# Kernel tuning notes

Measured on AMD Instinct MI355X. Metric: run time of the kernel, lower is better.

## Reference

```python
import jax, jax.numpy as jnp
import numpy as np

B, M, N, E = 64, 100, 6400, 102400   # graphs, nodes/graph, total nodes, edges
H, D, EMB, IMG, NC = 4, 512, 768, 1024, 2
HD = H * D
EPS = 1e-5


def _bn2(x, g, b, m, v):
    # BatchNorm1d eval mode on [B, C]
    return (x - m) / jnp.sqrt(v + EPS) * g + b


def _bn3(x, g, b, m, v):
    # BatchNorm1d eval mode on [B, C, L] -> channel dim is axis 1 (node index)
    return (x - m[None, :, None]) / jnp.sqrt(v + EPS)[None, :, None] * g[None, :, None] + b[None, :, None]


def _gat(feat, src, dst, W, al, ar, bias):
    # DGL GATConv (eval: feat_drop is identity). feat: [N, F_in]
    h = (feat @ W.T).reshape(-1, H, D)                 # [N, H, D]
    el = (h * al[None]).sum(-1)                         # [N, H]
    er = (h * ar[None]).sum(-1)                         # [N, H]
    e = jax.nn.leaky_relu(el[src] + er[dst], negative_slope=0.2)  # [E, H]
    mx = jax.ops.segment_max(e, dst, num_segments=N)
    a = jnp.exp(e - mx[dst])
    s = jax.ops.segment_sum(a, dst, num_segments=N)
    alpha = a / s[dst]                                  # edge softmax over incoming edges
    out = jax.ops.segment_sum(h[src] * alpha[:, :, None], dst, num_segments=N)  # [N, H, D]
    return out + bias.reshape(1, H, D)


def setup_inputs() -> dict:
    key = jax.random.key(0)
    ks = iter(jax.random.split(key, 80))
    n = lambda *s: jax.random.normal(next(ks), s, dtype=jnp.float32)

    def bn(c):
        return (1.0 + 0.1 * n(c), 0.1 * n(c), 0.1 * n(c),
                0.5 + jax.random.uniform(next(ks), (c,), dtype=jnp.float32))

    s = 0.02
    inp = {}
    inp['img_embedding'] = n(B, IMG)
    inp['func_text_embedding'] = n(B, EMB)
    inp['unix_emb'] = n(N, EMB)
    inp['pos_emb'] = jax.random.uniform(next(ks), (N, 4), dtype=jnp.float32)
    inp['src'] = jax.random.randint(next(ks), (E,), 0, N)
    inp['dst'] = jax.random.randint(next(ks), (E,), 0, N)
    inp['gat1_W'] = n(HD, EMB) * s; inp['gat1_al'] = n(H, D) * 0.1; inp['gat1_ar'] = n(H, D) * 0.1; inp['gat1_b'] = jnp.zeros(HD)
    inp['gat2_W'] = n(HD, HD) * s; inp['gat2_al'] = n(H, D) * 0.1; inp['gat2_ar'] = n(H, D) * 0.1; inp['gat2_b'] = jnp.zeros(HD)
    inp['fc_W'] = n(D, HD) * s; inp['fc_b'] = jnp.zeros(D)
    inp['hidden_W'] = n(8, D, D) * s; inp['hidden_b'] = jnp.zeros((8, D))
    inp['bn_text_g'], inp['bn_text_b'], inp['bn_text_m'], inp['bn_text_v'] = bn(EMB)
    inp['fc_text_W'] = n(D, EMB) * s; inp['fc_text_b'] = jnp.zeros(D)
    inp['swin_g'], inp['swin_b'], inp['swin_m'], inp['swin_v'] = bn(IMG)
    inp['swinfc_W'] = n(D, IMG) * s; inp['swinfc_b'] = jnp.zeros(D)
    inp['bngat_g'], inp['bngat_b'], inp['bngat_m'], inp['bngat_v'] = bn(M)
    inp['fc_gat_W'] = n(480, D) * s; inp['fc_gat_b'] = jnp.zeros(480)
    inp['bnbb_g'], inp['bnbb_b'], inp['bnbb_m'], inp['bnbb_v'] = bn(M)
    inp['fc_bbox_W'] = n(32, 4) * s; inp['fc_bbox_b'] = jnp.zeros(32)
    inp['fbn_g'], inp['fbn_b'], inp['fbn_m'], inp['fbn_v'] = bn(3 * D)
    inp['final_W'] = n(NC, 3 * D) * s; inp['final_b'] = jnp.zeros(NC)
    return inp


def reference(img_embedding, func_text_embedding, unix_emb, pos_emb, src, dst,
              gat1_W, gat1_al, gat1_ar, gat1_b, gat2_W, gat2_al, gat2_ar, gat2_b,
              fc_W, fc_b, hidden_W, hidden_b,
              bn_text_g, bn_text_b, bn_text_m, bn_text_v, fc_text_W, fc_text_b,
              swin_g, swin_b, swin_m, swin_v, swinfc_W, swinfc_b,
              bngat_g, bngat_b, bngat_m, bngat_v, fc_gat_W, fc_gat_b,
              bnbb_g, bnbb_b, bnbb_m, bnbb_v, fc_bbox_W, fc_bbox_b,
              fbn_g, fbn_b, fbn_m, fbn_v, final_W, final_b):
    # image branch
    x = jax.nn.elu(_bn2(img_embedding, swin_g, swin_b, swin_m, swin_v) @ swinfc_W.T + swinfc_b)
    # text branch
    ft = jax.nn.elu(_bn2(func_text_embedding, bn_text_g, bn_text_b, bn_text_m, bn_text_v) @ fc_text_W.T + fc_text_b)
    # graph branch: two stacked GATConv layers (dropout is identity in eval)
    h = _gat(unix_emb, src, dst, gat1_W, gat1_al, gat1_ar, gat1_b).reshape(N, HD)
    h = _gat(h, src, dst, gat2_W, gat2_al, gat2_ar, gat2_b).reshape(N, HD)
    h = jax.nn.elu(h @ fc_W.T + fc_b)
    for i in range(8):
        h = jax.nn.elu(h @ hidden_W[i].T + hidden_b[i])
    # unbatch + pad to max_node=100 -> pure reshape (all graphs have exactly M nodes)
    h_i = h.reshape(B, M, D)
    pos_i = pos_emb.reshape(B, M, 4)
    h_i = jax.nn.elu(_bn3(h_i, bngat_g, bngat_b, bngat_m, bngat_v) @ fc_gat_W.T + fc_gat_b)      # [B, M, 480]
    pos_i = jax.nn.elu(_bn3(pos_i, bnbb_g, bnbb_b, bnbb_m, bnbb_v) @ fc_bbox_W.T + fc_bbox_b)    # [B, M, 32]
    h_feature = jnp.concatenate([h_i, pos_i], axis=2).mean(axis=1)                                # [B, 512]
    all_feats = jnp.concatenate([x, h_feature, ft], axis=1)                                       # [B, 1536]
    return _bn2(all_feats, fbn_g, fbn_b, fbn_m, fbn_v) @ final_W.T + final_b
```

## Files before the change

### kernel.cpp

```cpp
#include <hip/hip_runtime.h>
#include <math.h>

#define Bg   64
#define Mg   100
#define Ng   6400
#define Eg   102400
#define Hh   4
#define Dd   512
#define HDd  2048
#define EMBd 768
#define IMGd 1024
#define EPSc 1e-5f

typedef __bf16 bf16x8 __attribute__((ext_vector_type(8)));
typedef float  f32x4  __attribute__((ext_vector_type(4)));

__device__ __forceinline__ float eluf(float x) { return x > 0.f ? x : expm1f(x); }

__device__ __forceinline__ unsigned short f2bf(float x) {
    unsigned int u = __builtin_bit_cast(unsigned int, x);
    u += 0x7FFFu + ((u >> 16) & 1u);
    return (unsigned short)(u >> 16);
}
__device__ __forceinline__ float bf2f(unsigned short s) {
    return __builtin_bit_cast(float, ((unsigned int)s) << 16);
}

__device__ __forceinline__ void gld16(const void* g, void* l) {
    __builtin_amdgcn_global_load_lds(
        (const __attribute__((address_space(1))) void*)g,
        (__attribute__((address_space(3))) void*)l, 16, 0, 0);
}

__global__ __launch_bounds__(256)
void gemm_bf16(const unsigned short* __restrict__ A,
               const unsigned short* __restrict__ W,
               const float* __restrict__ bias, void* __restrict__ C,
               int M, int N, int K, int act, int outbf)
{
    __shared__ __align__(16) unsigned short As[128 * 32];
    __shared__ __align__(16) unsigned short Bs[128 * 32];
    const int tid  = threadIdx.x;
    const int lane = tid & 63, wid = tid >> 6;
    const int bm = blockIdx.y * 128, bn = blockIdx.x * 128;
    const int wm = (wid >> 1) * 64, wn = (wid & 1) * 64;
    const int lrow = lane >> 2;
    const int lcol = (lane & 3) << 3;

    f32x4 acc[4][4] = {};

    const int ra = wid * 32;
    const unsigned short* gA0 = A + (size_t)(bm + ra + lrow) * K + lcol;
    const unsigned short* gA1 = A + (size_t)(bm + ra + 16 + lrow) * K + lcol;
    int rb0 = bn + ra + lrow;       if (rb0 >= N) rb0 = N - 1;
    int rb1 = bn + ra + 16 + lrow;  if (rb1 >= N) rb1 = N - 1;
    const unsigned short* gB0 = W + (size_t)rb0 * K + lcol;
    const unsigned short* gB1 = W + (size_t)rb1 * K + lcol;
    unsigned short* lA0 = &As[(ra)      * 32];
    unsigned short* lA1 = &As[(ra + 16) * 32];
    unsigned short* lB0 = &Bs[(ra)      * 32];
    unsigned short* lB1 = &Bs[(ra + 16) * 32];

    const int frow = lane & 15;
    const int quad = (lane >> 4) << 3;

    for (int k0 = 0; k0 < K; k0 += 32) {
        gld16(gA0 + k0, lA0);
        gld16(gA1 + k0, lA1);
        gld16(gB0 + k0, lB0);
        gld16(gB1 + k0, lB1);
        __syncthreads();
        bf16x8 af[4], bfr[4];
#pragma unroll
        for (int i = 0; i < 4; ++i)
            af[i]  = *(const bf16x8*)&As[(wm + i * 16 + frow) * 32 + quad];
#pragma unroll
        for (int i = 0; i < 4; ++i)
            bfr[i] = *(const bf16x8*)&Bs[(wn + i * 16 + frow) * 32 + quad];
#pragma unroll
        for (int mi = 0; mi < 4; ++mi)
#pragma unroll
            for (int ni = 0; ni < 4; ++ni)
                acc[mi][ni] = __builtin_amdgcn_mfma_f32_16x16x32_bf16(
                    af[mi], bfr[ni], acc[mi][ni], 0, 0, 0);
        __syncthreads();
    }

    const int crow0 = bm + wm + ((lane >> 4) << 2);
    const int ccol0 = bn + wn + (lane & 15);
#pragma unroll
    for (int mi = 0; mi < 4; ++mi) {
#pragma unroll
        for (int ni = 0; ni < 4; ++ni) {
            int col = ccol0 + ni * 16;
            if (col >= N) continue;
            float bv = bias ? bias[col] : 0.f;
#pragma unroll
            for (int r = 0; r < 4; ++r) {
                int row = crow0 + mi * 16 + r;
                float v = acc[mi][ni][r] + bv;
                if (act) v = eluf(v);
                if (outbf) ((unsigned short*)C)[(size_t)row * N + col] = f2bf(v);
                else       ((float*)C)[(size_t)row * N + col] = v;
            }
        }
    }
}

__global__ __launch_bounds__(256)
void gemm_bf16_t64(const unsigned short* __restrict__ A,
                   const unsigned short* __restrict__ W,
                   const float* __restrict__ bias, void* __restrict__ C,
                   int M, int N, int K, int act, int outbf)
{
    __shared__ __align__(16) unsigned short As[64 * 32];
    __shared__ __align__(16) unsigned short Bs[64 * 32];
    const int tid  = threadIdx.x;
    const int lane = tid & 63, wid = tid >> 6;
    const int bm = blockIdx.y * 64, bn = blockIdx.x * 64;
    const int wm = (wid >> 1) * 32, wn = (wid & 1) * 32;
    const int lrow = lane >> 2;
    const int lcol = (lane & 3) << 3;

    f32x4 acc[2][2] = {};

    const int ra = wid * 16;
    const unsigned short* gA = A + (size_t)(bm + ra + lrow) * K + lcol;
    int rb = bn + ra + lrow; if (rb >= N) rb = N - 1;
    const unsigned short* gB = W + (size_t)rb * K + lcol;
    unsigned short* lA = &As[ra * 32];
    unsigned short* lB = &Bs[ra * 32];

    const int frow = lane & 15;
    const int quad = (lane >> 4) << 3;

    for (int k0 = 0; k0 < K; k0 += 32) {
        gld16(gA + k0, lA);
        gld16(gB + k0, lB);
        __syncthreads();
        bf16x8 af0 = *(const bf16x8*)&As[(wm + frow) * 32 + quad];
        bf16x8 af1 = *(const bf16x8*)&As[(wm + 16 + frow) * 32 + quad];
        bf16x8 bf0 = *(const bf16x8*)&Bs[(wn + frow) * 32 + quad];
        bf16x8 bf1 = *(const bf16x8*)&Bs[(wn + 16 + frow) * 32 + quad];
        acc[0][0] = __builtin_amdgcn_mfma_f32_16x16x32_bf16(af0, bf0, acc[0][0], 0, 0, 0);
        acc[0][1] = __builtin_amdgcn_mfma_f32_16x16x32_bf16(af0, bf1, acc[0][1], 0, 0, 0);
        acc[1][0] = __builtin_amdgcn_mfma_f32_16x16x32_bf16(af1, bf0, acc[1][0], 0, 0, 0);
        acc[1][1] = __builtin_amdgcn_mfma_f32_16x16x32_bf16(af1, bf1, acc[1][1], 0, 0, 0);
        __syncthreads();
    }

    const int crow0 = bm + wm + ((lane >> 4) << 2);
    const int ccol0 = bn + wn + (lane & 15);
#pragma unroll
    for (int mi = 0; mi < 2; ++mi) {
#pragma unroll
        for (int ni = 0; ni < 2; ++ni) {
            int col = ccol0 + ni * 16;
            if (col >= N) continue;
            float bv = bias ? bias[col] : 0.f;
#pragma unroll
            for (int r = 0; r < 4; ++r) {
                int row = crow0 + mi * 16 + r;
                float v = acc[mi][ni][r] + bv;
                if (act) v = eluf(v);
                if (outbf) ((unsigned short*)C)[(size_t)row * N + col] = f2bf(v);
                else       ((float*)C)[(size_t)row * N + col] = v;
            }
        }
    }
}

__global__ __launch_bounds__(256)
void gemm_nt(const float* __restrict__ A, const float* __restrict__ W,
             const float* __restrict__ bias, float* __restrict__ C,
             int M, int N, int K, int act)
{
    __shared__ float As[16 * 68];
    __shared__ float Ws[16 * 68];
    const int tid = threadIdx.x;
    const int tx = tid & 15, ty = tid >> 4;
    const int bm = blockIdx.y * 64, bn = blockIdx.x * 64;
    const int lrow = tid >> 2;
    const int lk4  = (tid & 3) << 2;
    const int arow = bm + lrow;
    const int wrow = bn + lrow;
    const float* Aptr = A + (size_t)arow * K + lk4;
    const float* Wptr = W + (size_t)wrow * K + lk4;
    float acc[4][4] = {{0.f,0.f,0.f,0.f},{0.f,0.f,0.f,0.f},{0.f,0.f,0.f,0.f},{0.f,0.f,0.f,0.f}};

    for (int k0 = 0; k0 < K; k0 += 16) {
        float4 av = make_float4(0.f,0.f,0.f,0.f);
        float4 wv = make_float4(0.f,0.f,0.f,0.f);
        if (arow < M) av = *(const float4*)(Aptr + k0);
        if (wrow < N) wv = *(const float4*)(Wptr + k0);
        As[(lk4+0)*68 + lrow] = av.x;
        As[(lk4+1)*68 + lrow] = av.y;
        As[(lk4+2)*68 + lrow] = av.z;
        As[(lk4+3)*68 + lrow] = av.w;
        Ws[(lk4+0)*68 + lrow] = wv.x;
        Ws[(lk4+1)*68 + lrow] = wv.y;
        Ws[(lk4+2)*68 + lrow] = wv.z;
        Ws[(lk4+3)*68 + lrow] = wv.w;
        __syncthreads();
#pragma unroll
        for (int kk = 0; kk < 16; ++kk) {
            float4 a = *(const float4*)&As[kk*68 + (ty<<2)];
            float4 w = *(const float4*)&Ws[kk*68 + (tx<<2)];
            acc[0][0] += a.x*w.x; acc[0][1] += a.x*w.y; acc[0][2] += a.x*w.z; acc[0][3] += a.x*w.w;
            acc[1][0] += a.y*w.x; acc[1][1] += a.y*w.y; acc[1][2] += a.y*w.z; acc[1][3] += a.y*w.w;
            acc[2][0] += a.z*w.x; acc[2][1] += a.z*w.y; acc[2][2] += a.z*w.z; acc[2][3] += a.z*w.w;
            acc[3][0] += a.w*w.x; acc[3][1] += a.w*w.y; acc[3][2] += a.w*w.z; acc[3][3] += a.w*w.w;
        }
        __syncthreads();
    }

#pragma unroll
    for (int i = 0; i < 4; ++i) {
        int row = bm + (ty<<2) + i;
        int col = bn + (tx<<2);
        if (row < M && col < N) {
            float4 v;
            v.x = acc[i][0]; v.y = acc[i][1]; v.z = acc[i][2]; v.w = acc[i][3];
            if (bias) { v.x += bias[col]; v.y += bias[col+1]; v.z += bias[col+2]; v.w += bias[col+3]; }
            if (act == 1) { v.x = eluf(v.x); v.y = eluf(v.y); v.z = eluf(v.z); v.w = eluf(v.w); }
            *(float4*)(C + (size_t)row * N + col) = v;
        }
    }
}

struct CvtPack {
    const float* s[6];
    unsigned short* d[6];
    int n4[6];
};

__global__ void cvt_all(CvtPack p, int total4)
{
    int i = blockIdx.x * 256 + threadIdx.x;
    if (i >= total4) return;
#pragma unroll
    for (int k = 0; k < 6; ++k) {
        if (i < p.n4[k]) {
            float4 v = ((const float4*)p.s[k])[i];
            ushort4 o;
            o.x = f2bf(v.x); o.y = f2bf(v.y); o.z = f2bf(v.z); o.w = f2bf(v.w);
            ((ushort4*)p.d[k])[i] = o;
            return;
        }
        i -= p.n4[k];
    }
}

__global__ void bn_col(const float* __restrict__ x, const float* __restrict__ g,
                       const float* __restrict__ b, const float* __restrict__ m,
                       const float* __restrict__ v, float* __restrict__ y,
                       int rows, int cols)
{
    int i = blockIdx.x * 256 + threadIdx.x;
    if (i >= rows * cols) return;
    int c = i % cols;
    float inv = rsqrtf(v[c] + EPSc);
    y[i] = (x[i] - m[c]) * inv * g[c] + b[c];
}

__global__ void bn_node_b4(const ushort4* __restrict__ x, const float* __restrict__ g,
                           const float* __restrict__ b, const float* __restrict__ m,
                           const float* __restrict__ v, ushort4* __restrict__ y,
                           int total4, int Cdim4)
{
    int i = blockIdx.x * 256 + threadIdx.x;
    if (i >= total4) return;
    int n = i / Cdim4;
    int p = n % Mg;
    float sc = rsqrtf(v[p] + EPSc) * g[p];
    float sh = b[p] - m[p] * sc;
    ushort4 xv = x[i];
    ushort4 o;
    o.x = f2bf(bf2f(xv.x) * sc + sh);
    o.y = f2bf(bf2f(xv.y) * sc + sh);
    o.z = f2bf(bf2f(xv.z) * sc + sh);
    o.w = f2bf(bf2f(xv.w) * sc + sh);
    y[i] = o;
}

__global__ void zero_i32(int* __restrict__ p, int n)
{
    int i = blockIdx.x * 256 + threadIdx.x;
    if (i < n) p[i] = 0;
}

__global__ void count_dst(const int* __restrict__ dst, int* __restrict__ counts, int E)
{
    int i = blockIdx.x * 256 + threadIdx.x;
    if (i < E) atomicAdd(&counts[dst[i]], 1);
}

__global__ __launch_bounds__(1024)
void scan_excl(const int* __restrict__ counts, int* __restrict__ offs,
               int* __restrict__ cursor, int n)
{
    __shared__ int sm[1024];
    __shared__ int carry;
    if (threadIdx.x == 0) carry = 0;
    __syncthreads();
    for (int base = 0; base < n; base += 1024) {
        int i = base + (int)threadIdx.x;
        int v = (i < n) ? counts[i] : 0;
        sm[threadIdx.x] = v;
        __syncthreads();
        for (int o = 1; o < 1024; o <<= 1) {
            int t = (threadIdx.x >= (unsigned)o) ? sm[threadIdx.x - o] : 0;
            __syncthreads();
            sm[threadIdx.x] += t;
            __syncthreads();
        }
        int incl = sm[threadIdx.x];
        int myc = carry;
        if (i < n) {
            int ex = myc + incl - v;
            offs[i] = ex;
            cursor[i] = ex;
        }
        __syncthreads();
        if (threadIdx.x == 1023) carry = myc + sm[1023];
        __syncthreads();
    }
    if (threadIdx.x == 0) offs[n] = carry;
}

__global__ void scatter_edges(const int* __restrict__ dst, int* __restrict__ cursor,
                              int* __restrict__ eid, int E)
{
    int i = blockIdx.x * 256 + threadIdx.x;
    if (i < E) {
        int p = atomicAdd(&cursor[dst[i]], 1);
        eid[p] = i;
    }
}

__global__ __launch_bounds__(256)
void elr_kernel(const unsigned short* __restrict__ Hm, const float* __restrict__ al,
                const float* __restrict__ ar, float* __restrict__ el,
                float* __restrict__ er)
{
    int wid = threadIdx.x >> 6, lane = threadIdx.x & 63;
    int g = (blockIdx.x << 2) + wid;
    int n = g >> 2, h = g & 3;
    const unsigned short* hp = Hm + ((size_t)n << 11) + (h << 9) + (lane << 3);
    const float* alp = al + (h << 9) + (lane << 3);
    const float* arp = ar + (h << 9) + (lane << 3);
    ushort4 x0 = *(const ushort4*)hp;
    ushort4 x1 = *(const ushort4*)(hp + 4);
    float4 l0 = *(const float4*)alp, l1 = *(const float4*)(alp + 4);
    float4 r0 = *(const float4*)arp, r1 = *(const float4*)(arp + 4);
    float a0 = bf2f(x0.x), a1 = bf2f(x0.y), a2 = bf2f(x0.z), a3 = bf2f(x0.w);
    float a4 = bf2f(x1.x), a5 = bf2f(x1.y), a6 = bf2f(x1.z), a7 = bf2f(x1.w);
    float se = a0*l0.x + a1*l0.y + a2*l0.z + a3*l0.w + a4*l1.x + a5*l1.y + a6*l1.z + a7*l1.w;
    float sr = a0*r0.x + a1*r0.y + a2*r0.z + a3*r0.w + a4*r1.x + a5*r1.y + a6*r1.z + a7*r1.w;
#pragma unroll
    for (int o = 32; o > 0; o >>= 1) {
        se += __shfl_down(se, o, 64);
        sr += __shfl_down(sr, o, 64);
    }
    if (lane == 0) { el[g] = se; er[g] = sr; }
}

__global__ __launch_bounds__(256)
void gat_agg(const unsigned short* __restrict__ Hm, const float* __restrict__ el,
             const float* __restrict__ er, const int* __restrict__ src,
             const int* __restrict__ offs, const int* __restrict__ eid,
             const float* __restrict__ bias, unsigned short* __restrict__ out)
{
    int n = blockIdx.x;
    int tid = threadIdx.x;
    int beg = offs[n], end = offs[n + 1];
    int deg = end - beg;
    const int b0 = tid << 2;
    const int b1 = 1024 + (tid << 2);
    const int h0 = tid >> 7;
    const int h1 = h0 + 2;

    if (deg == 0) {
#pragma unroll
        for (int j = 0; j < 4; ++j) {
            out[((size_t)n << 11) + b0 + j] = f2bf(bias[b0 + j]);
            out[((size_t)n << 11) + b1 + j] = f2bf(bias[b1 + j]);
        }
        return;
    }

    __shared__ float m_sh[4], s_sh[4], al_sh[4];
    __shared__ int   src_sh[128];
    __shared__ float logit_sh[512];
    __shared__ float w_sh[512];

    if (tid < 4) { m_sh[tid] = -INFINITY; s_sh[tid] = 0.f; }
    float acc[8] = {0.f,0.f,0.f,0.f,0.f,0.f,0.f,0.f};
    __syncthreads();

    for (int c0 = 0; c0 < deg; c0 += 128) {
        int cnt = min(128, deg - c0);
        for (int i = tid; i < cnt; i += 256) src_sh[i] = src[eid[beg + c0 + i]];
        __syncthreads();
        for (int idx = tid; idx < (cnt << 2); idx += 256) {
            int i = idx >> 2, h = idx & 3;
            float x = el[(src_sh[i] << 2) + h] + er[(n << 2) + h];
            logit_sh[idx] = x > 0.f ? x : 0.2f * x;
        }
        __syncthreads();
        if (tid < 4) {
            float cm = -INFINITY;
            for (int i = 0; i < cnt; ++i) cm = fmaxf(cm, logit_sh[(i << 2) + tid]);
            float mn = fmaxf(m_sh[tid], cm);
            al_sh[tid] = expf(m_sh[tid] - mn);
            m_sh[tid] = mn;
        }
        __syncthreads();
        for (int idx = tid; idx < (cnt << 2); idx += 256)
            w_sh[idx] = expf(logit_sh[idx] - m_sh[idx & 3]);
        __syncthreads();
        if (tid < 4) {
            float cs = 0.f;
            for (int i = 0; i < cnt; ++i) cs += w_sh[(i << 2) + tid];
            s_sh[tid] = s_sh[tid] * al_sh[tid] + cs;
        }
        float r0 = al_sh[h0], r1 = al_sh[h1];
        acc[0] *= r0; acc[1] *= r0; acc[2] *= r0; acc[3] *= r0;
        acc[4] *= r1; acc[5] *= r1; acc[6] *= r1; acc[7] *= r1;
        for (int i = 0; i < cnt; ++i) {
            const unsigned short* hp = Hm + ((size_t)src_sh[i] << 11);
            ushort4 a = *(const ushort4*)(hp + b0);
            ushort4 b = *(const ushort4*)(hp + b1);
            float w0 = w_sh[(i << 2) + h0], w1 = w_sh[(i << 2) + h1];
            acc[0] += w0 * bf2f(a.x); acc[1] += w0 * bf2f(a.y);
            acc[2] += w0 * bf2f(a.z); acc[3] += w0 * bf2f(a.w);
            acc[4] += w1 * bf2f(b.x); acc[5] += w1 * bf2f(b.y);
            acc[6] += w1 * bf2f(b.z); acc[7] += w1 * bf2f(b.w);
        }
        __syncthreads();
    }

    float is0 = 1.f / s_sh[h0], is1 = 1.f / s_sh[h1];
#pragma unroll
    for (int j = 0; j < 4; ++j) {
        out[((size_t)n << 11) + b0 + j] = f2bf(acc[j] * is0 + bias[b0 + j]);
        out[((size_t)n << 11) + b1 + j] = f2bf(acc[4 + j] * is1 + bias[b1 + j]);
    }
}

__global__ void mean_kernel(const float* __restrict__ hg, const float* __restrict__ pos,
                            const float* __restrict__ bg, const float* __restrict__ bb_,
                            const float* __restrict__ bm_, const float* __restrict__ bv_,
                            const float* __restrict__ W, const float* __restrict__ bias,
                            float* __restrict__ hf)
{
    int i = blockIdx.x * 256 + threadIdx.x;
    if (i >= Bg * Dd) return;
    int bb = i >> 9, c = i & 511;
    float s = 0.f;
    if (c < 480) {
        const float* p = hg + (size_t)bb * Mg * 480 + c;
        for (int mm = 0; mm < Mg; ++mm) s += p[mm * 480];
    } else {
        int o = c - 480;
        float w0 = W[(o << 2) + 0], w1 = W[(o << 2) + 1];
        float w2 = W[(o << 2) + 2], w3 = W[(o << 2) + 3];
        float bo = bias[o];
        const float* pp = pos + (size_t)bb * Mg * 4;
        for (int mm = 0; mm < Mg; ++mm) {
            float sc = rsqrtf(bv_[mm] + EPSc) * bg[mm];
            float sh = bb_[mm] - bm_[mm] * sc;
            float a = bo + (pp[mm*4+0]*sc+sh)*w0 + (pp[mm*4+1]*sc+sh)*w1
                         + (pp[mm*4+2]*sc+sh)*w2 + (pp[mm*4+3]*sc+sh)*w3;
            s += eluf(a);
        }
    }
    hf[i] = s * 0.01f;
}

__global__ __launch_bounds__(256)
void final_kernel(const float* __restrict__ x, const float* __restrict__ hf,
                  const float* __restrict__ ft, const float* __restrict__ g,
                  const float* __restrict__ b, const float* __restrict__ m,
                  const float* __restrict__ v, const float* __restrict__ W,
                  const float* __restrict__ bias, float* __restrict__ out)
{
    int bb = blockIdx.x;
    int tid = threadIdx.x;
    float a0 = 0.f, a1 = 0.f;
    for (int c = tid; c < 1536; c += 256) {
        float xv = (c < 512) ? x[bb * 512 + c]
                 : (c < 1024) ? hf[bb * 512 + (c - 512)]
                              : ft[bb * 512 + (c - 1024)];
        float z = (xv - m[c]) * rsqrtf(v[c] + EPSc) * g[c] + b[c];
        a0 += z * W[c];
        a1 += z * W[1536 + c];
    }
    __shared__ float r0[256], r1[256];
    r0[tid] = a0; r1[tid] = a1;
    __syncthreads();
    for (int o = 128; o > 0; o >>= 1) {
        if (tid < o) { r0[tid] += r0[tid + o]; r1[tid] += r1[tid + o]; }
        __syncthreads();
    }
    if (tid == 0) {
        out[bb * 2 + 0] = r0[0] + bias[0];
        out[bb * 2 + 1] = r1[0] + bias[1];
    }
}

extern "C" void kernel_launch(void* const* d_in, const int* in_sizes, int n_in,
                              void* d_out, int out_size, void* d_ws, size_t ws_size,
                              hipStream_t stream)
{
    (void)in_sizes; (void)n_in; (void)out_size; (void)ws_size;

    const float* img   = (const float*)d_in[0];
    const float* ftxt  = (const float*)d_in[1];
    const float* unixe = (const float*)d_in[2];
    const float* pos   = (const float*)d_in[3];
    const int*   src   = (const int*)  d_in[4];
    const int*   dst   = (const int*)  d_in[5];
    const float* g1W   = (const float*)d_in[6];
    const float* g1al  = (const float*)d_in[7];
    const float* g1ar  = (const float*)d_in[8];
    const float* g1b   = (const float*)d_in[9];
    const float* g2W   = (const float*)d_in[10];
    const float* g2al  = (const float*)d_in[11];
    const float* g2ar  = (const float*)d_in[12];
    const float* g2b   = (const float*)d_in[13];
    const float* fcW   = (const float*)d_in[14];
    const float* fcb   = (const float*)d_in[15];
    const float* hidW  = (const float*)d_in[16];
    const float* hidb  = (const float*)d_in[17];
    const float* btg   = (const float*)d_in[18];
    const float* btb   = (const float*)d_in[19];
    const float* btm   = (const float*)d_in[20];
    const float* btv   = (const float*)d_in[21];
    const float* ftW   = (const float*)d_in[22];
    const float* ftbi  = (const float*)d_in[23];
    const float* swg   = (const float*)d_in[24];
    const float* swb   = (const float*)d_in[25];
    const float* swm   = (const float*)d_in[26];
    const float* swv   = (const float*)d_in[27];
    const float* swW   = (const float*)d_in[28];
    const float* swbi  = (const float*)d_in[29];
    const float* bgg   = (const float*)d_in[30];
    const float* bgb   = (const float*)d_in[31];
    const float* bgm   = (const float*)d_in[32];
    const float* bgv   = (const float*)d_in[33];
    const float* fgW   = (const float*)d_in[34];
    const float* fgb   = (const float*)d_in[35];
    const float* bbgp  = (const float*)d_in[36];
    const float* bbbp  = (const float*)d_in[37];
    const float* bbmp  = (const float*)d_in[38];
    const float* bbvp  = (const float*)d_in[39];
    const float* fbW   = (const float*)d_in[40];
    const float* fbb   = (const float*)d_in[41];
    const float* fng   = (const float*)d_in[42];
    const float* fnb   = (const float*)d_in[43];
    const float* fnm   = (const float*)d_in[44];
    const float* fnv   = (const float*)d_in[45];
    const float* fiW   = (const float*)d_in[46];
    const float* fib   = (const float*)d_in[47];
    float* out = (float*)d_out;

    char* p = (char*)d_ws;
    unsigned short* fA  = (unsigned short*)p; p += (size_t)Ng * HDd * 2;
    unsigned short* fB  = (unsigned short*)p; p += (size_t)Ng * HDd * 2;
    unsigned short* fC  = (unsigned short*)p; p += (size_t)Ng * Dd * 2;
    unsigned short* fD  = (unsigned short*)p; p += (size_t)Ng * Dd * 2;
    float*          fE  = (float*)p;          p += (size_t)Ng * 480 * 4;
    float*          el  = (float*)p;          p += (size_t)Ng * Hh * 4;
    float*          er  = (float*)p;          p += (size_t)Ng * Hh * 4;
    float*          xb  = (float*)p;          p += (size_t)Bg * Dd * 4;
    float*          ftb = (float*)p;          p += (size_t)Bg * Dd * 4;
    float*          hf  = (float*)p;          p += (size_t)Bg * Dd * 4;
    float*          ti  = (float*)p;          p += (size_t)Bg * IMGd * 4;
    float*          tt  = (float*)p;          p += (size_t)Bg * EMBd * 4;
    unsigned short* ubf = (unsigned short*)p; p += (size_t)Ng * EMBd * 2;
    unsigned short* wg1 = (unsigned short*)p; p += (size_t)HDd * EMBd * 2;
    unsigned short* wg2 = (unsigned short*)p; p += (size_t)HDd * HDd * 2;
    unsigned short* wfc = (unsigned short*)p; p += (size_t)Dd * HDd * 2;
    unsigned short* whid= (unsigned short*)p; p += (size_t)8 * Dd * Dd * 2;
    unsigned short* wfg = (unsigned short*)p; p += (size_t)480 * Dd * 2;
    int* counts = (int*)p; p += (size_t)Ng * 4;
    int* offs   = (int*)p; p += (size_t)(Ng + 1) * 4 + 12;
    int* cursor = (int*)p; p += (size_t)Ng * 4;
    int* eid    = (int*)p; p += (size_t)Eg * 4;

    CvtPack cp;
    cp.s[0] = unixe; cp.d[0] = ubf;  cp.n4[0] = Ng * EMBd / 4;
    cp.s[1] = g1W;   cp.d[1] = wg1;  cp.n4[1] = HDd * EMBd / 4;
    cp.s[2] = g2W;   cp.d[2] = wg2;  cp.n4[2] = HDd * HDd / 4;
    cp.s[3] = fcW;   cp.d[3] = wfc;  cp.n4[3] = Dd * HDd / 4;
    cp.s[4] = hidW;  cp.d[4] = whid; cp.n4[4] = 8 * Dd * Dd / 4;
    cp.s[5] = fgW;   cp.d[5] = wfg;  cp.n4[5] = 480 * Dd / 4;
    int total4 = cp.n4[0] + cp.n4[1] + cp.n4[2] + cp.n4[3] + cp.n4[4] + cp.n4[5];
    cvt_all<<<(total4 + 255)/256, 256, 0, stream>>>(cp, total4);

    bn_col<<<(Bg*IMGd + 255)/256, 256, 0, stream>>>(img, swg, swb, swm, swv, ti, Bg, IMGd);
    gemm_nt<<<dim3(8, 1), 256, 0, stream>>>(ti, swW, swbi, xb, Bg, Dd, IMGd, 1);
    bn_col<<<(Bg*EMBd + 255)/256, 256, 0, stream>>>(ftxt, btg, btb, btm, btv, tt, Bg, EMBd);
    gemm_nt<<<dim3(8, 1), 256, 0, stream>>>(tt, ftW, ftbi, ftb, Bg, Dd, EMBd, 1);

    zero_i32<<<(Ng + 255)/256, 256, 0, stream>>>(counts, Ng);
    count_dst<<<(Eg + 255)/256, 256, 0, stream>>>(dst, counts, Eg);
    scan_excl<<<1, 1024, 0, stream>>>(counts, offs, cursor, Ng);
    scatter_edges<<<(Eg + 255)/256, 256, 0, stream>>>(dst, cursor, eid, Eg);

    gemm_bf16<<<dim3(HDd/128, Ng/128), 256, 0, stream>>>(ubf, wg1, nullptr, fA, Ng, HDd, EMBd, 0, 1);
    elr_kernel<<<Ng, 256, 0, stream>>>(fA, g1al, g1ar, el, er);
    gat_agg<<<Ng, 256, 0, stream>>>(fA, el, er, src, offs, eid, g1b, fB);

    gemm_bf16<<<dim3(HDd/128, Ng/128), 256, 0, stream>>>(fB, wg2, nullptr, fA, Ng, HDd, HDd, 0, 1);
    elr_kernel<<<Ng, 256, 0, stream>>>(fA, g2al, g2ar, el, er);
    gat_agg<<<Ng, 256, 0, stream>>>(fA, el, er, src, offs, eid, g2b, fB);

    gemm_bf16_t64<<<dim3(Dd/64, Ng/64), 256, 0, stream>>>(fB, wfc, fcb, fC, Ng, Dd, HDd, 1, 1);

    unsigned short* cur = fC; unsigned short* nxt = fD;
    for (int i = 0; i < 8; ++i) {
        gemm_bf16_t64<<<dim3(Dd/64, Ng/64), 256, 0, stream>>>(
            cur, whid + (size_t)i * Dd * Dd, hidb + (size_t)i * Dd, nxt, Ng, Dd, Dd, 1, 1);
        unsigned short* t = cur; cur = nxt; nxt = t;
    }

    bn_node_b4<<<(Ng*Dd/4 + 255)/256, 256, 0, stream>>>(
        (const ushort4*)cur, bgg, bgb, bgm, bgv, (ushort4*)nxt, Ng*Dd/4, Dd/4);
    gemm_bf16_t64<<<dim3(8, Ng/64), 256, 0, stream>>>(nxt, wfg, fgb, fE, Ng, 480, Dd, 1, 0);

    mean_kernel<<<(Bg*Dd + 255)/256, 256, 0, stream>>>(fE, pos, bbgp, bbbp, bbmp, bbvp, fbW, fbb, hf);

    final_kernel<<<Bg, 256, 0, stream>>>(xb, hf, ftb, fng, fnb, fnm, fnv, fiW, fib, out);
}
```

Measured before the change: 850.3 us.

## Fuse fc, eight hidden layers, node BN and fc_gat into one persistent MLP kernel

Replaces the fc GEMM, the eight hidden-layer GEMMs, the node-wise batchnorm pass and the fc_gat GEMM with a single kernel. Each block owns 64 rows, keeps the activations in LDS across all layers and streams full 512-wide weight tiles with double buffering. The batchnorm is folded algebraically into the last GEMM's epilogue using precomputed row sums of the fp32 fc_gat weights. This removes ten launches and the round trips of intermediate activations through global memory. In exchange only 100 blocks run with one block per CU, so occupancy is low and weights are reloaded by every block.

New measurement: 966.5 us. 1.14x slower.

```diff
diff --git a/kernel.cpp b/kernel.cpp
--- a/kernel.cpp
+++ b/kernel.cpp
@@ -11,6 +11,9 @@
 #define EMBd 768
 #define IMGd 1024
 #define EPSc 1e-5f
+
+#define MROWS 64
+#define APAD  520
 
 typedef __bf16 bf16x8 __attribute__((ext_vector_type(8)));
 typedef float  f32x4  __attribute__((ext_vector_type(4)));
@@ -107,67 +110,188 @@
     }
 }
 
-__global__ __launch_bounds__(256)
-void gemm_bf16_t64(const unsigned short* __restrict__ A,
-                   const unsigned short* __restrict__ W,
-                   const float* __restrict__ bias, void* __restrict__ C,
-                   int M, int N, int K, int act, int outbf)
-{
-    __shared__ __align__(16) unsigned short As[64 * 32];
-    __shared__ __align__(16) unsigned short Bs[64 * 32];
+__global__ __launch_bounds__(256, 1)
+void mega_mlp(const unsigned short* __restrict__ Ain,
+              const unsigned short* __restrict__ Wfc,
+              const float* __restrict__ bfc,
+              const unsigned short* __restrict__ Whid,
+              const float* __restrict__ bhid,
+              const unsigned short* __restrict__ Wfg,
+              const float* __restrict__ bfg,
+              const float* __restrict__ wsum,
+              const float* __restrict__ bng, const float* __restrict__ bnb,
+              const float* __restrict__ bnm, const float* __restrict__ bnv,
+              float* __restrict__ Eout)
+{
+    extern __shared__ __align__(16) unsigned short smem[];
+    unsigned short* act = smem;
+    unsigned short* Wb0 = act + MROWS * APAD;
+    unsigned short* Wb1 = Wb0 + 512 * 32;
+    unsigned short* Ab0 = Wb1 + 512 * 32;
+    unsigned short* Ab1 = Ab0 + MROWS * 32;
+    unsigned short* Wb[2] = { Wb0, Wb1 };
+    unsigned short* Ab[2] = { Ab0, Ab1 };
+
     const int tid  = threadIdx.x;
     const int lane = tid & 63, wid = tid >> 6;
-    const int bm = blockIdx.y * 64, bn = blockIdx.x * 64;
-    const int wm = (wid >> 1) * 32, wn = (wid & 1) * 32;
-    const int lrow = lane >> 2;
-    const int lcol = (lane & 3) << 3;
-
-    f32x4 acc[2][2] = {};
-
-    const int ra = wid * 16;
-    const unsigned short* gA = A + (size_t)(bm + ra + lrow) * K + lcol;
-    int rb = bn + ra + lrow; if (rb >= N) rb = N - 1;
-    const unsigned short* gB = W + (size_t)rb * K + lcol;
-    unsigned short* lA = &As[ra * 32];
-    unsigned short* lB = &Bs[ra * 32];
-
+    const int bm   = blockIdx.x * MROWS;
+    const int wn   = wid * 128;
     const int frow = lane & 15;
     const int quad = (lane >> 4) << 3;
-
-    for (int k0 = 0; k0 < K; k0 += 32) {
-        gld16(gA + k0, lA);
-        gld16(gB + k0, lB);
-        __syncthreads();
-        bf16x8 af0 = *(const bf16x8*)&As[(wm + frow) * 32 + quad];
-        bf16x8 af1 = *(const bf16x8*)&As[(wm + 16 + frow) * 32 + quad];
-        bf16x8 bf0 = *(const bf16x8*)&Bs[(wn + frow) * 32 + quad];
-        bf16x8 bf1 = *(const bf16x8*)&Bs[(wn + 16 + frow) * 32 + quad];
-        acc[0][0] = __builtin_amdgcn_mfma_f32_16x16x32_bf16(af0, bf0, acc[0][0], 0, 0, 0);
-        acc[0][1] = __builtin_amdgcn_mfma_f32_16x16x32_bf16(af0, bf1, acc[0][1], 0, 0, 0);
-        acc[1][0] = __builtin_amdgcn_mfma_f32_16x16x32_bf16(af1, bf0, acc[1][0], 0, 0, 0);
-        acc[1][1] = __builtin_amdgcn_mfma_f32_16x16x32_bf16(af1, bf1, acc[1][1], 0, 0, 0);
-        __syncthreads();
-    }
-
-    const int crow0 = bm + wm + ((lane >> 4) << 2);
-    const int ccol0 = bn + wn + (lane & 15);
-#pragma unroll
-    for (int mi = 0; mi < 2; ++mi) {
-#pragma unroll
-        for (int ni = 0; ni < 2; ++ni) {
-            int col = ccol0 + ni * 16;
-            if (col >= N) continue;
-            float bv = bias ? bias[col] : 0.f;
+    const int rsub = (lane >> 4) << 2;
+
+    auto stageW = [&](const unsigned short* Wsrc, int Ks, int Nrows, int k0, int buf) {
+#pragma unroll
+        for (int j = 0; j < 8; ++j) {
+            int s = j * 256 + tid;
+            int row = s >> 2, grp = s & 3;
+            if (row >= Nrows) row = Nrows - 1;
+            gld16(Wsrc + (size_t)row * Ks + k0 + grp * 8,
+                  &Wb[buf][(size_t)(j * 256 + wid * 64) * 8]);
+        }
+    };
+    auto stageA = [&](int k0, int buf) {
+        int row = tid >> 2, grp = tid & 3;
+        gld16(Ain + (size_t)(bm + row) * HDd + k0 + grp * 8,
+              &Ab[buf][(size_t)(wid * 64) * 8]);
+    };
+
+    {
+        f32x4 acc[4][8] = {};
+        stageA(0, 0);
+        stageW(Wfc, HDd, 512, 0, 0);
+        int c = 0;
+        for (int it = 0; it < HDd / 32; ++it) {
+            __syncthreads();
+            if (it + 1 < HDd / 32) {
+                stageA((it + 1) * 32, c ^ 1);
+                stageW(Wfc, HDd, 512, (it + 1) * 32, c ^ 1);
+            }
+            bf16x8 af[4], bfr[8];
+#pragma unroll
+            for (int mi = 0; mi < 4; ++mi)
+                af[mi] = *(const bf16x8*)&Ab[c][(mi * 16 + frow) * 32 + quad];
+#pragma unroll
+            for (int ni = 0; ni < 8; ++ni)
+                bfr[ni] = *(const bf16x8*)&Wb[c][(wn + ni * 16 + frow) * 32 + quad];
+#pragma unroll
+            for (int mi = 0; mi < 4; ++mi)
+#pragma unroll
+                for (int ni = 0; ni < 8; ++ni)
+                    acc[mi][ni] = __builtin_amdgcn_mfma_f32_16x16x32_bf16(
+                        af[mi], bfr[ni], acc[mi][ni], 0, 0, 0);
+            c ^= 1;
+        }
+        __syncthreads();
+#pragma unroll
+        for (int mi = 0; mi < 4; ++mi)
+#pragma unroll
+            for (int ni = 0; ni < 8; ++ni) {
+                int col = wn + ni * 16 + frow;
+                float bv = bfc[col];
+#pragma unroll
+                for (int r = 0; r < 4; ++r) {
+                    int row = mi * 16 + rsub + r;
+                    act[row * APAD + col] = f2bf(eluf(acc[mi][ni][r] + bv));
+                }
+            }
+    }
+
+    for (int L = 0; L < 8; ++L) {
+        const unsigned short* Wl = Whid + (size_t)L * Dd * Dd;
+        const float* bl = bhid + L * Dd;
+        f32x4 acc[4][8] = {};
+        stageW(Wl, Dd, 512, 0, 0);
+        int c = 0;
+        for (int it = 0; it < Dd / 32; ++it) {
+            __syncthreads();
+            if (it + 1 < Dd / 32) stageW(Wl, Dd, 512, (it + 1) * 32, c ^ 1);
+            bf16x8 af[4], bfr[8];
+#pragma unroll
+            for (int mi = 0; mi < 4; ++mi)
+                af[mi] = *(const bf16x8*)&act[(mi * 16 + frow) * APAD + it * 32 + quad];
+#pragma unroll
+            for (int ni = 0; ni < 8; ++ni)
+                bfr[ni] = *(const bf16x8*)&Wb[c][(wn + ni * 16 + frow) * 32 + quad];
+#pragma unroll
+            for (int mi = 0; mi < 4; ++mi)
+#pragma unroll
+                for (int ni = 0; ni < 8; ++ni)
+                    acc[mi][ni] = __builtin_amdgcn_mfma_f32_16x16x32_bf16(
+                        af[mi], bfr[ni], acc[mi][ni], 0, 0, 0);
+            c ^= 1;
+        }
+        __syncthreads();
+#pragma unroll
+        for (int mi = 0; mi < 4; ++mi)
+#pragma unroll
+            for (int ni = 0; ni < 8; ++ni) {
+                int col = wn + ni * 16 + frow;
+                float bv = bl[col];
+#pragma unroll
+                for (int r = 0; r < 4; ++r) {
+                    int row = mi * 16 + rsub + r;
+                    act[row * APAD + col] = f2bf(eluf(acc[mi][ni][r] + bv));
+                }
+            }
+    }
+
+    {
+        f32x4 acc[4][8] = {};
+        stageW(Wfg, Dd, 480, 0, 0);
+        int c = 0;
+        for (int it = 0; it < Dd / 32; ++it) {
+            __syncthreads();
+            if (it + 1 < Dd / 32) stageW(Wfg, Dd, 480, (it + 1) * 32, c ^ 1);
+            bf16x8 af[4], bfr[8];
+#pragma unroll
+            for (int mi = 0; mi < 4; ++mi)
+                af[mi] = *(const bf16x8*)&act[(mi * 16 + frow) * APAD + it * 32 + quad];
+#pragma unroll
+            for (int ni = 0; ni < 8; ++ni)
+                bfr[ni] = *(const bf16x8*)&Wb[c][(wn + ni * 16 + frow) * 32 + quad];
+#pragma unroll
+            for (int mi = 0; mi < 4; ++mi)
+#pragma unroll
+                for (int ni = 0; ni < 8; ++ni)
+                    acc[mi][ni] = __builtin_amdgcn_mfma_f32_16x16x32_bf16(
+                        af[mi], bfr[ni], acc[mi][ni], 0, 0, 0);
+            c ^= 1;
+        }
+#pragma unroll
+        for (int mi = 0; mi < 4; ++mi) {
 #pragma unroll
             for (int r = 0; r < 4; ++r) {
-                int row = crow0 + mi * 16 + r;
-                float v = acc[mi][ni][r] + bv;
-                if (act) v = eluf(v);
-                if (outbf) ((unsigned short*)C)[(size_t)row * N + col] = f2bf(v);
-                else       ((float*)C)[(size_t)row * N + col] = v;
+                int lrow = mi * 16 + rsub + r;
+                int grow = bm + lrow;
+                int p = grow % Mg;
+                float sc = rsqrtf(bnv[p] + EPSc) * bng[p];
+                float sh = bnb[p] - bnm[p] * sc;
+#pragma unroll
+                for (int ni = 0; ni < 8; ++ni) {
+                    int col = wn + ni * 16 + frow;
+                    if (col < 480) {
+                        float v = sc * acc[mi][ni][r] + sh * wsum[col] + bfg[col];
+                        Eout[(size_t)grow * 480 + col] = eluf(v);
+                    }
+                }
             }
         }
     }
+}
+
+__global__ __launch_bounds__(256)
+void wsum_kernel(const float* __restrict__ W, float* __restrict__ s)
+{
+    int row = (blockIdx.x << 2) + (threadIdx.x >> 6);
+    int lane = threadIdx.x & 63;
+    if (row >= 480) return;
+    const float* p = W + (size_t)row * Dd;
+    float a = 0.f;
+    for (int k = lane; k < Dd; k += 64) a += p[k];
+#pragma unroll
+    for (int o = 32; o > 0; o >>= 1) a += __shfl_down(a, o, 64);
+    if (lane == 0) s[row] = a;
 }
 
 __global__ __launch_bounds__(256)
@@ -261,26 +385,6 @@
     int c = i % cols;
     float inv = rsqrtf(v[c] + EPSc);
     y[i] = (x[i] - m[c]) * inv * g[c] + b[c];
-}
-
-__global__ void bn_node_b4(const ushort4* __restrict__ x, const float* __restrict__ g,
-                           const float* __restrict__ b, const float* __restrict__ m,
-                           const float* __restrict__ v, ushort4* __restrict__ y,
-                           int total4, int Cdim4)
-{
-    int i = blockIdx.x * 256 + threadIdx.x;
-    if (i >= total4) return;
-    int n = i / Cdim4;
-    int p = n % Mg;
-    float sc = rsqrtf(v[p] + EPSc) * g[p];
-    float sh = b[p] - m[p] * sc;
-    ushort4 xv = x[i];
-    ushort4 o;
-    o.x = f2bf(bf2f(xv.x) * sc + sh);
-    o.y = f2bf(bf2f(xv.y) * sc + sh);
-    o.z = f2bf(bf2f(xv.z) * sc + sh);
-    o.w = f2bf(bf2f(xv.w) * sc + sh);
-    y[i] = o;
 }
 
 __global__ void zero_i32(int* __restrict__ p, int n)
@@ -568,8 +672,6 @@
     char* p = (char*)d_ws;
     unsigned short* fA  = (unsigned short*)p; p += (size_t)Ng * HDd * 2;
     unsigned short* fB  = (unsigned short*)p; p += (size_t)Ng * HDd * 2;
-    unsigned short* fC  = (unsigned short*)p; p += (size_t)Ng * Dd * 2;
-    unsigned short* fD  = (unsigned short*)p; p += (size_t)Ng * Dd * 2;
     float*          fE  = (float*)p;          p += (size_t)Ng * 480 * 4;
     float*          el  = (float*)p;          p += (size_t)Ng * Hh * 4;
     float*          er  = (float*)p;          p += (size_t)Ng * Hh * 4;
@@ -578,6 +680,7 @@
     float*          hf  = (float*)p;          p += (size_t)Bg * Dd * 4;
     float*          ti  = (float*)p;          p += (size_t)Bg * IMGd * 4;
     float*          tt  = (float*)p;          p += (size_t)Bg * EMBd * 4;
+    float*          wsm = (float*)p;          p += (size_t)480 * 4;
     unsigned short* ubf = (unsigned short*)p; p += (size_t)Ng * EMBd * 2;
     unsigned short* wg1 = (unsigned short*)p; p += (size_t)HDd * EMBd * 2;
     unsigned short* wg2 = (unsigned short*)p; p += (size_t)HDd * HDd * 2;
@@ -598,6 +701,7 @@
     cp.s[5] = fgW;   cp.d[5] = wfg;  cp.n4[5] = 480 * Dd / 4;
     int total4 = cp.n4[0] + cp.n4[1] + cp.n4[2] + cp.n4[3] + cp.n4[4] + cp.n4[5];
     cvt_all<<<(total4 + 255)/256, 256, 0, stream>>>(cp, total4);
+    wsum_kernel<<<120, 256, 0, stream>>>(fgW, wsm);
 
     bn_col<<<(Bg*IMGd + 255)/256, 256, 0, stream>>>(img, swg, swb, swm, swv, ti, Bg, IMGd);
     gemm_nt<<<dim3(8, 1), 256, 0, stream>>>(ti, swW, swbi, xb, Bg, Dd, IMGd, 1);
@@ -617,18 +721,9 @@
     elr_kernel<<<Ng, 256, 0, stream>>>(fA, g2al, g2ar, el, er);
     gat_agg<<<Ng, 256, 0, stream>>>(fA, el, er, src, offs, eid, g2b, fB);
 
-    gemm_bf16_t64<<<dim3(Dd/64, Ng/64), 256, 0, stream>>>(fB, wfc, fcb, fC, Ng, Dd, HDd, 1, 1);
-
-    unsigned short* cur = fC; unsigned short* nxt = fD;
-    for (int i = 0; i < 8; ++i) {
-        gemm_bf16_t64<<<dim3(Dd/64, Ng/64), 256, 0, stream>>>(
-            cur, whid + (size_t)i * Dd * Dd, hidb + (size_t)i * Dd, nxt, Ng, Dd, Dd, 1, 1);
-        unsigned short* t = cur; cur = nxt; nxt = t;
-    }
-
-    bn_node_b4<<<(Ng*Dd/4 + 255)/256, 256, 0, stream>>>(
-        (const ushort4*)cur, bgg, bgb, bgm, bgv, (ushort4*)nxt, Ng*Dd/4, Dd/4);
-    gemm_bf16_t64<<<dim3(8, Ng/64), 256, 0, stream>>>(nxt, wfg, fgb, fE, Ng, 480, Dd, 1, 0);
+    size_t smem = (size_t)(MROWS * APAD + 2 * 512 * 32 + 2 * MROWS * 32) * 2;
+    mega_mlp<<<Ng / MROWS, 256, smem, stream>>>(
+        fB, wfc, fcb, whid, hidb, wfg, fgb, wsm, bgg, bgb, bgm, bgv, fE);
 
     mean_kernel<<<(Bg*Dd + 255)/256, 256, 0, stream>>>(fE, pos, bbgp, bbbp, bbmp, bbvp, fbW, fbb, hf);
 
```

## Fold node batchnorm into fc_gat GEMM epilogue, rewrite scan and mean kernels

Applied to the files above, without the earlier changes.

Removes the separate per-node BatchNorm pass over the bf16 hidden activations. The per-row scale is now applied inside a new GEMM epilogue, and the shift is handled algebraically through precomputed row sums of the fc_gat weight. The single-block exclusive scan is rewritten to give each thread 7 elements and use wave shuffles instead of the iterated shared-memory Hillis-Steele loop. The mean kernel is remapped to one block per graph. The folded BN uses fp32 weight sums while the GEMM uses bf16 weights, which slightly changes rounding.

Result: slower. 868.5 us (+2.1%).

```diff
diff --git a/kernel.cpp b/kernel.cpp
--- a/kernel.cpp
+++ b/kernel.cpp
@@ -168,6 +168,86 @@
             }
         }
     }
+}
+
+__global__ __launch_bounds__(256)
+void gemm_t64_fcgat(const unsigned short* __restrict__ A,
+                    const unsigned short* __restrict__ W,
+                    const float* __restrict__ bfg, const float* __restrict__ wsum,
+                    const float* __restrict__ bng, const float* __restrict__ bnb,
+                    const float* __restrict__ bnm, const float* __restrict__ bnv,
+                    float* __restrict__ Eout, int M, int N, int K)
+{
+    __shared__ __align__(16) unsigned short As[64 * 32];
+    __shared__ __align__(16) unsigned short Bs[64 * 32];
+    const int tid  = threadIdx.x;
+    const int lane = tid & 63, wid = tid >> 6;
+    const int bm = blockIdx.y * 64, bn = blockIdx.x * 64;
+    const int wm = (wid >> 1) * 32, wn = (wid & 1) * 32;
+    const int lrow = lane >> 2;
+    const int lcol = (lane & 3) << 3;
+
+    f32x4 acc[2][2] = {};
+
+    const int ra = wid * 16;
+    const unsigned short* gA = A + (size_t)(bm + ra + lrow) * K + lcol;
+    int rb = bn + ra + lrow; if (rb >= N) rb = N - 1;
+    const unsigned short* gB = W + (size_t)rb * K + lcol;
+    unsigned short* lA = &As[ra * 32];
+    unsigned short* lB = &Bs[ra * 32];
+
+    const int frow = lane & 15;
+    const int quad = (lane >> 4) << 3;
+
+    for (int k0 = 0; k0 < K; k0 += 32) {
+        gld16(gA + k0, lA);
+        gld16(gB + k0, lB);
+        __syncthreads();
+        bf16x8 af0 = *(const bf16x8*)&As[(wm + frow) * 32 + quad];
+        bf16x8 af1 = *(const bf16x8*)&As[(wm + 16 + frow) * 32 + quad];
+        bf16x8 bf0 = *(const bf16x8*)&Bs[(wn + frow) * 32 + quad];
+        bf16x8 bf1 = *(const bf16x8*)&Bs[(wn + 16 + frow) * 32 + quad];
+        acc[0][0] = __builtin_amdgcn_mfma_f32_16x16x32_bf16(af0, bf0, acc[0][0], 0, 0, 0);
+        acc[0][1] = __builtin_amdgcn_mfma_f32_16x16x32_bf16(af0, bf1, acc[0][1], 0, 0, 0);
+        acc[1][0] = __builtin_amdgcn_mfma_f32_16x16x32_bf16(af1, bf0, acc[1][0], 0, 0, 0);
+        acc[1][1] = __builtin_amdgcn_mfma_f32_16x16x32_bf16(af1, bf1, acc[1][1], 0, 0, 0);
+        __syncthreads();
+    }
+
+    const int crow0 = bm + wm + ((lane >> 4) << 2);
+    const int ccol0 = bn + wn + (lane & 15);
+#pragma unroll
+    for (int mi = 0; mi < 2; ++mi) {
+#pragma unroll
+        for (int r = 0; r < 4; ++r) {
+            int row = crow0 + mi * 16 + r;
+            int p = row % Mg;
+            float sc = rsqrtf(bnv[p] + EPSc) * bng[p];
+            float sh = bnb[p] - bnm[p] * sc;
+#pragma unroll
+            for (int ni = 0; ni < 2; ++ni) {
+                int col = ccol0 + ni * 16;
+                if (col < N) {
+                    float v = sc * acc[mi][ni][r] + sh * wsum[col] + bfg[col];
+                    Eout[(size_t)row * N + col] = eluf(v);
+                }
+            }
+        }
+    }
+}
+
+__global__ __launch_bounds__(256)
+void wsum_kernel(const float* __restrict__ W, float* __restrict__ s)
+{
+    int row = (blockIdx.x << 2) + (threadIdx.x >> 6);
+    int lane = threadIdx.x & 63;
+    if (row >= 480) return;
+    const float* p = W + (size_t)row * Dd;
+    float a = 0.f;
+    for (int k = lane; k < Dd; k += 64) a += p[k];
+#pragma unroll
+    for (int o = 32; o > 0; o >>= 1) a += __shfl_down(a, o, 64);
+    if (lane == 0) s[row] = a;
 }
 
 __global__ __launch_bounds__(256)
@@ -263,26 +343,6 @@
     y[i] = (x[i] - m[c]) * inv * g[c] + b[c];
 }
 
-__global__ void bn_node_b4(const ushort4* __restrict__ x, const float* __restrict__ g,
-                           const float* __restrict__ b, const float* __restrict__ m,
-                           const float* __restrict__ v, ushort4* __restrict__ y,
-                           int total4, int Cdim4)
-{
-    int i = blockIdx.x * 256 + threadIdx.x;
-    if (i >= total4) return;
-    int n = i / Cdim4;
-    int p = n % Mg;
-    float sc = rsqrtf(v[p] + EPSc) * g[p];
-    float sh = b[p] - m[p] * sc;
-    ushort4 xv = x[i];
-    ushort4 o;
-    o.x = f2bf(bf2f(xv.x) * sc + sh);
-    o.y = f2bf(bf2f(xv.y) * sc + sh);
-    o.z = f2bf(bf2f(xv.z) * sc + sh);
-    o.w = f2bf(bf2f(xv.w) * sc + sh);
-    y[i] = o;
-}
-
 __global__ void zero_i32(int* __restrict__ p, int n)
 {
     int i = blockIdx.x * 256 + threadIdx.x;
@@ -299,33 +359,41 @@
 void scan_excl(const int* __restrict__ counts, int* __restrict__ offs,
                int* __restrict__ cursor, int n)
 {
-    __shared__ int sm[1024];
-    __shared__ int carry;
-    if (threadIdx.x == 0) carry = 0;
+    const int T = 7;
+    int tid = threadIdx.x;
+    int base = tid * T;
+    int v[T];
+    int tot = 0;
+#pragma unroll
+    for (int j = 0; j < T; ++j) {
+        int i = base + j;
+        v[j] = (i < n) ? counts[i] : 0;
+        tot += v[j];
+    }
+    int lane = tid & 63, w = tid >> 6;
+    int incl = tot;
+#pragma unroll
+    for (int o = 1; o < 64; o <<= 1) {
+        int t = __shfl_up(incl, o, 64);
+        if (lane >= o) incl += t;
+    }
+    __shared__ int wtot[16];
+    __shared__ int wbase[16];
+    if (lane == 63) wtot[w] = incl;
     __syncthreads();
-    for (int base = 0; base < n; base += 1024) {
-        int i = base + (int)threadIdx.x;
-        int v = (i < n) ? counts[i] : 0;
-        sm[threadIdx.x] = v;
-        __syncthreads();
-        for (int o = 1; o < 1024; o <<= 1) {
-            int t = (threadIdx.x >= (unsigned)o) ? sm[threadIdx.x - o] : 0;
-            __syncthreads();
-            sm[threadIdx.x] += t;
-            __syncthreads();
-        }
-        int incl = sm[threadIdx.x];
-        int myc = carry;
-        if (i < n) {
-            int ex = myc + incl - v;
-            offs[i] = ex;
-            cursor[i] = ex;
-        }
-        __syncthreads();
-        if (threadIdx.x == 1023) carry = myc + sm[1023];
-        __syncthreads();
-    }
-    if (threadIdx.x == 0) offs[n] = carry;
+    if (tid == 0) {
+        int s = 0;
+        for (int i = 0; i < 16; ++i) { wbase[i] = s; s += wtot[i]; }
+    }
+    __syncthreads();
+    int ex = wbase[w] + incl - tot;
+#pragma unroll
+    for (int j = 0; j < T; ++j) {
+        int i = base + j;
+        if (i < n) { offs[i] = ex; cursor[i] = ex; }
+        ex += v[j];
+    }
+    if (tid == 1023) offs[n] = ex;
 }
 
 __global__ void scatter_edges(const int* __restrict__ dst, int* __restrict__ cursor,
@@ -448,34 +516,39 @@
     }
 }
 
-__global__ void mean_kernel(const float* __restrict__ hg, const float* __restrict__ pos,
-                            const float* __restrict__ bg, const float* __restrict__ bb_,
-                            const float* __restrict__ bm_, const float* __restrict__ bv_,
-                            const float* __restrict__ W, const float* __restrict__ bias,
-                            float* __restrict__ hf)
-{
-    int i = blockIdx.x * 256 + threadIdx.x;
-    if (i >= Bg * Dd) return;
-    int bb = i >> 9, c = i & 511;
-    float s = 0.f;
-    if (c < 480) {
-        const float* p = hg + (size_t)bb * Mg * 480 + c;
-        for (int mm = 0; mm < Mg; ++mm) s += p[mm * 480];
-    } else {
-        int o = c - 480;
+__global__ __launch_bounds__(256)
+void mean_kernel(const float* __restrict__ hg, const float* __restrict__ pos,
+                 const float* __restrict__ bg, const float* __restrict__ bb_,
+                 const float* __restrict__ bm_, const float* __restrict__ bv_,
+                 const float* __restrict__ W, const float* __restrict__ bias,
+                 float* __restrict__ hf)
+{
+    int bb = blockIdx.x;
+    int tid = threadIdx.x;
+    int c0 = tid, c1 = tid + 256;
+    const float* hb = hg + (size_t)bb * Mg * 480;
+    float s0 = 0.f, s1 = 0.f;
+    for (int m = 0; m < Mg; ++m) {
+        s0 += hb[m * 480 + c0];
+        if (c1 < 480) s1 += hb[m * 480 + c1];
+    }
+    if (c1 >= 480) {
+        int o = c1 - 480;
         float w0 = W[(o << 2) + 0], w1 = W[(o << 2) + 1];
         float w2 = W[(o << 2) + 2], w3 = W[(o << 2) + 3];
         float bo = bias[o];
         const float* pp = pos + (size_t)bb * Mg * 4;
-        for (int mm = 0; mm < Mg; ++mm) {
-            float sc = rsqrtf(bv_[mm] + EPSc) * bg[mm];
-            float sh = bb_[mm] - bm_[mm] * sc;
-            float a = bo + (pp[mm*4+0]*sc+sh)*w0 + (pp[mm*4+1]*sc+sh)*w1
-                         + (pp[mm*4+2]*sc+sh)*w2 + (pp[mm*4+3]*sc+sh)*w3;
-            s += eluf(a);
-        }
-    }
-    hf[i] = s * 0.01f;
+        s1 = 0.f;
+        for (int m = 0; m < Mg; ++m) {
+            float sc = rsqrtf(bv_[m] + EPSc) * bg[m];
+            float sh = bb_[m] - bm_[m] * sc;
+            float a = bo + (pp[m*4+0]*sc+sh)*w0 + (pp[m*4+1]*sc+sh)*w1
+                         + (pp[m*4+2]*sc+sh)*w2 + (pp[m*4+3]*sc+sh)*w3;
+            s1 += eluf(a);
+        }
+    }
+    hf[bb * 512 + c0] = s0 * 0.01f;
+    hf[bb * 512 + c1] = s1 * 0.01f;
 }
 
 __global__ __launch_bounds__(256)
@@ -578,6 +651,7 @@
     float*          hf  = (float*)p;          p += (size_t)Bg * Dd * 4;
     float*          ti  = (float*)p;          p += (size_t)Bg * IMGd * 4;
     float*          tt  = (float*)p;          p += (size_t)Bg * EMBd * 4;
+    float*          wsm = (float*)p;          p += (size_t)480 * 4;
     unsigned short* ubf = (unsigned short*)p; p += (size_t)Ng * EMBd * 2;
     unsigned short* wg1 = (unsigned short*)p; p += (size_t)HDd * EMBd * 2;
     unsigned short* wg2 = (unsigned short*)p; p += (size_t)HDd * HDd * 2;
@@ -598,6 +672,7 @@
     cp.s[5] = fgW;   cp.d[5] = wfg;  cp.n4[5] = 480 * Dd / 4;
     int total4 = cp.n4[0] + cp.n4[1] + cp.n4[2] + cp.n4[3] + cp.n4[4] + cp.n4[5];
     cvt_all<<<(total4 + 255)/256, 256, 0, stream>>>(cp, total4);
+    wsum_kernel<<<120, 256, 0, stream>>>(fgW, wsm);
 
     bn_col<<<(Bg*IMGd + 255)/256, 256, 0, stream>>>(img, swg, swb, swm, swv, ti, Bg, IMGd);
     gemm_nt<<<dim3(8, 1), 256, 0, stream>>>(ti, swW, swbi, xb, Bg, Dd, IMGd, 1);
@@ -626,11 +701,10 @@
         unsigned short* t = cur; cur = nxt; nxt = t;
     }
 
-    bn_node_b4<<<(Ng*Dd/4 + 255)/256, 256, 0, stream>>>(
-        (const ushort4*)cur, bgg, bgb, bgm, bgv, (ushort4*)nxt, Ng*Dd/4, Dd/4);
-    gemm_bf16_t64<<<dim3(8, Ng/64), 256, 0, stream>>>(nxt, wfg, fgb, fE, Ng, 480, Dd, 1, 0);
-
-    mean_kernel<<<(Bg*Dd + 255)/256, 256, 0, stream>>>(fE, pos, bbgp, bbbp, bbmp, bbvp, fbW, fbb, hf);
+    gemm_t64_fcgat<<<dim3(8, Ng/64), 256, 0, stream>>>(
+        cur, wfg, fgb, wsm, bgg, bgb, bgm, bgv, fE, Ng, 480, Dd);
+
+    mean_kernel<<<Bg, 256, 0, stream>>>(fE, pos, bbgp, bbbp, bbmp, bbvp, fbW, fbb, hf);
 
     final_kernel<<<Bg, 256, 0, stream>>>(xb, hf, ftb, fng, fnb, fnm, fnv, fiW, fib, out);
 }
```
